# Kernel tuning notes

Measured on AMD Instinct MI355X. Metric: run time of the kernel, lower is better.

Reference implementation:

```python
import jax, jax.numpy as jnp
import numpy as np

B, N, C = 32, 256, 4096
H = 16
HEAD_DIM = C // H  # 256 == N, required by the module's math
SCALE = HEAD_DIM ** -0.5


def setup_inputs() -> dict:
    key = jax.random.key(0)
    ks = jax.random.split(key, 7)
    std = C ** -0.5
    return {
        "x1": jax.random.normal(ks[0], (B, N, C), dtype=jnp.float32),
        "x2": jax.random.normal(ks[1], (B, N, C), dtype=jnp.float32),
        "Wq": jax.random.normal(ks[2], (C, C), dtype=jnp.float32) * std,
        "Wk": jax.random.normal(ks[3], (C, C), dtype=jnp.float32) * std,
        "Wv": jax.random.normal(ks[4], (C, C), dtype=jnp.float32) * std,
        "Wp": jax.random.normal(ks[5], (C, C), dtype=jnp.float32) * std,
        "bp": jnp.zeros((C,), dtype=jnp.float32),
    }


def reference(x1, x2, Wq, Wk, Wv, Wp, bp):
    b, n, c = x1.shape
    h, hd = H, HEAD_DIM
    # QKV projections (qkv_bias=False); q pre-scaled as in source
    q = (x1 @ Wq.T) * SCALE
    k = x2 @ Wk.T
    v = x2 @ Wv.T
    split = lambda t: t.reshape(b, n, h, hd).transpose(0, 2, 1, 3)  # b h n hd
    q, k, v = split(q), split(k), split(v)
    # channel-wise attention: q^T @ k over the token axis -> [b, h, hd, hd]
    attn = jax.nn.softmax(jnp.einsum("bhni,bhnj->bhij", q, k), axis=-1)
    # attn @ v: inner dim of attn (hd) contracts with token axis of v (n == hd)
    out = jnp.einsum("bhin,bhnc->bhic", attn, v)  # [b, h, hd, hd]
    out = out.transpose(0, 2, 1, 3).reshape(b, n, c)
    x = out @ Wp.T + bp
    return (x, attn)
```

## Files before the change

### kernel.cpp

```cpp
#include <hip/hip_runtime.h>

typedef __attribute__((ext_vector_type(4))) float f32x4;
typedef __attribute__((ext_vector_type(8))) short short8;
typedef __attribute__((ext_vector_type(4))) unsigned short ushort4v;

__device__ __forceinline__ unsigned short rne_bf16(float f) {
  unsigned int u = __builtin_bit_cast(unsigned int, f);
  u += 0x7FFFu + ((u >> 16) & 1u);
  return (unsigned short)(u >> 16);
}

__device__ __forceinline__ void async16(void* lds, const void* g) {
  __builtin_amdgcn_global_load_lds(
      (const __attribute__((address_space(1))) void*)g,
      (__attribute__((address_space(3))) void*)lds, 16, 0, 0);
}

__device__ __forceinline__ f32x4 mfma16(short8 a, short8 b, f32x4 c) {
  return __builtin_amdgcn_mfma_f32_16x16x32_bf16(a, b, c, 0, 0, 0);
}

__global__ __launch_bounds__(256) void cast_k(const float* __restrict__ in,
                                              unsigned short* __restrict__ out,
                                              int n4) {
  int stride = gridDim.x * 256;
  for (int i = blockIdx.x * 256 + threadIdx.x; i < n4; i += stride) {
    float4 v = ((const float4*)in)[i];
    ushort4v o = {rne_bf16(v.x), rne_bf16(v.y), rne_bf16(v.z), rne_bf16(v.w)};
    ((ushort4v*)out)[i] = o;
  }
}

template <int MODE>
__global__ __launch_bounds__(512, 2) void gemm256(const unsigned short* __restrict__ A,
                                                  const unsigned short* __restrict__ B,
                                                  float* __restrict__ outF,
                                                  unsigned short* __restrict__ outB,
                                                  const float* __restrict__ bias,
                                                  int K, int lda, int ldb,
                                                  float scale, int gx) {
  __shared__ unsigned short lds[65536];
  const int tid = threadIdx.x;
  const int lane = tid & 63;
  const int wid = tid >> 6;
  const int wm = wid >> 2;
  const int wn = wid & 3;
  int lin = blockIdx.x;
  lin = (lin & 7) * (gridDim.x >> 3) + (lin >> 3);
  const int bx = lin % gx;
  const int by = lin / gx;
  const int m0 = by * 256, n0 = bx * 256;
  const int NT = K >> 6;

  const int gsw8 = (((tid & 3) ^ ((tid >> 3) & 3))) * 8;
  const unsigned short* gA = A + (size_t)(m0 + (tid >> 2)) * lda + gsw8;
  const unsigned short* gB = B + (size_t)(n0 + (tid >> 2)) * ldb + gsw8;
  const size_t astep = (size_t)128 * lda;
  const size_t bstep = (size_t)128 * ldb;
  unsigned short* ld0 = &lds[tid * 8];

#define STG_A(kt, kh, bf) do { \
    const unsigned short* s_ = gA + (kt) + (kh) * 32; \
    unsigned short* d_ = ld0 + (bf) * 32768 + (kh) * 8192; \
    async16(d_, s_); async16(d_ + 4096, s_ + astep); } while (0)
#define STG_B(kt, kh, bf) do { \
    const unsigned short* s_ = gB + (kt) + (kh) * 32; \
    unsigned short* d_ = ld0 + 16384 + (bf) * 32768 + (kh) * 8192; \
    async16(d_, s_); async16(d_ + 4096, s_ + bstep); } while (0)

  const int rl = lane & 15;
  const int ch = (lane >> 4) ^ ((rl >> 1) & 3);
  const int aidx = wm * 4096 + rl * 32 + ch * 8;
  const int bidx = 16384 + wn * 2048 + rl * 32 + ch * 8;

  f32x4 acc[8][4];
#pragma unroll
  for (int r = 0; r < 8; ++r)
#pragma unroll
    for (int s = 0; s < 4; ++s) acc[r][s] = (f32x4){0.f, 0.f, 0.f, 0.f};

  STG_A(0, 0, 0); STG_B(0, 0, 0); STG_A(0, 1, 0); STG_B(0, 1, 0);
  if (NT > 1) {
    STG_A(64, 0, 1); STG_B(64, 0, 1); STG_A(64, 1, 1);
    asm volatile("s_waitcnt vmcnt(6)" ::: "memory");
  } else {
    asm volatile("s_waitcnt vmcnt(0)" ::: "memory");
  }
  __builtin_amdgcn_s_barrier();

  short8 af[8];
  for (int t = 0; t < NT; ++t) {
    const int bb = (t & 1) * 32768;
    {
      short8 b0 = *(const short8*)&lds[bb + bidx];
      short8 b1 = *(const short8*)&lds[bb + bidx + 512];
#pragma unroll
      for (int r = 0; r < 8; ++r) af[r] = *(const short8*)&lds[bb + aidx + r * 512];
      if (t + 1 < NT) STG_B((t + 1) * 64, 1, (t + 1) & 1);
      __builtin_amdgcn_s_barrier();
      asm volatile("s_waitcnt lgkmcnt(0)" ::: "memory");
      __builtin_amdgcn_s_setprio(1);
#pragma unroll
      for (int r = 0; r < 8; ++r) {
        acc[r][0] = mfma16(af[r], b0, acc[r][0]);
        acc[r][1] = mfma16(af[r], b1, acc[r][1]);
      }
      __builtin_amdgcn_s_setprio(0);
      __builtin_amdgcn_s_barrier();
    }
    {
      short8 b2 = *(const short8*)&lds[bb + bidx + 1024];
      short8 b3 = *(const short8*)&lds[bb + bidx + 1536];
      if (t + 2 < NT) STG_A((t + 2) * 64, 0, t & 1);
      __builtin_amdgcn_s_barrier();
      asm volatile("s_waitcnt lgkmcnt(0)" ::: "memory");
      __builtin_amdgcn_s_setprio(1);
#pragma unroll
      for (int r = 0; r < 8; ++r) {
        acc[r][2] = mfma16(af[r], b2, acc[r][2]);
        acc[r][3] = mfma16(af[r], b3, acc[r][3]);
      }
      __builtin_amdgcn_s_setprio(0);
      __builtin_amdgcn_s_barrier();
    }
    {
      short8 b0 = *(const short8*)&lds[bb + 8192 + bidx];
      short8 b1 = *(const short8*)&lds[bb + 8192 + bidx + 512];
#pragma unroll
      for (int r = 0; r < 8; ++r) af[r] = *(const short8*)&lds[bb + 8192 + aidx + r * 512];
      if (t + 2 < NT) STG_B((t + 2) * 64, 0, t & 1);
      __builtin_amdgcn_s_barrier();
      asm volatile("s_waitcnt lgkmcnt(0)" ::: "memory");
      __builtin_amdgcn_s_setprio(1);
#pragma unroll
      for (int r = 0; r < 8; ++r) {
        acc[r][0] = mfma16(af[r], b0, acc[r][0]);
        acc[r][1] = mfma16(af[r], b1, acc[r][1]);
      }
      __builtin_amdgcn_s_setprio(0);
      __builtin_amdgcn_s_barrier();
    }
    {
      short8 b2 = *(const short8*)&lds[bb + 8192 + bidx + 1024];
      short8 b3 = *(const short8*)&lds[bb + 8192 + bidx + 1536];
      if (t + 2 < NT) STG_A((t + 2) * 64, 1, t & 1);
      __builtin_amdgcn_s_barrier();
      asm volatile("s_waitcnt lgkmcnt(0)" ::: "memory");
      __builtin_amdgcn_s_setprio(1);
#pragma unroll
      for (int r = 0; r < 8; ++r) {
        acc[r][2] = mfma16(af[r], b2, acc[r][2]);
        acc[r][3] = mfma16(af[r], b3, acc[r][3]);
      }
      __builtin_amdgcn_s_setprio(0);
      if (t + 1 < NT) {
        if (t + 1 == NT - 1) asm volatile("s_waitcnt vmcnt(0)" ::: "memory");
        else                 asm volatile("s_waitcnt vmcnt(6)" ::: "memory");
      }
      __builtin_amdgcn_s_barrier();
    }
  }
#undef STG_A
#undef STG_B

  const int fcol = lane & 15;
  const int frow = (lane >> 4) * 4;
#pragma unroll
  for (int r = 0; r < 8; ++r) {
#pragma unroll
    for (int s = 0; s < 4; ++s) {
      f32x4 v = acc[r][s];
      const int m = m0 + wm * 128 + r * 16 + frow;
      const int n = n0 + wn * 64 + s * 16 + fcol;
      if (MODE == 0) {
        ushort4v p;
#pragma unroll
        for (int j = 0; j < 4; ++j) p[j] = rne_bf16(v[j] * scale);
        size_t d = ((size_t)((m >> 8) * 16 + (n >> 8))) * 65536 +
                   (size_t)(n & 255) * 256 + (m & 255);
        *(ushort4v*)&outB[d] = p;
      } else {
        float bv = bias[n];
#pragma unroll
        for (int j = 0; j < 4; ++j) outF[(size_t)(m + j) * 4096 + n] = v[j] + bv;
      }
    }
  }
}

template <int MODE>
__global__ __launch_bounds__(256) void gemm_bt(const unsigned short* __restrict__ Ab,
                                               const unsigned short* __restrict__ Bb,
                                               float* __restrict__ outF,
                                               unsigned short* __restrict__ outB,
                                               int K, int lda, int ldb) {
  __shared__ short Ash[128 * 32];
  __shared__ short Bsh[128 * 32];

  const int tid = threadIdx.x;
  const int lane = tid & 63;
  const int wid = tid >> 6;
  const int z = blockIdx.z;
  const int m0 = blockIdx.y * 128;
  const int n0 = blockIdx.x * 128;

  const unsigned short* A = Ab + (size_t)z * 65536;
  const unsigned short* B = Bb + (size_t)z * 65536;

  const int wm = (wid >> 1) * 64;
  const int wn = (wid & 1) * 64;
  const int fcol = lane & 15;
  const int kslot = (lane >> 4) * 8;

  f32x4 acc[4][4];
#pragma unroll
  for (int r = 0; r < 4; ++r)
#pragma unroll
    for (int s = 0; s < 4; ++s) acc[r][s] = (f32x4){0.f, 0.f, 0.f, 0.f};

  const int arow = tid >> 2;
  const int acol = (tid & 3) * 8;
  const unsigned short* gA = A + (size_t)(m0 + arow) * lda + acol;
  const unsigned short* gB = B + (size_t)(n0 + arow) * ldb + acol;
  short* lA = &Ash[tid * 8];
  short* lB = &Bsh[tid * 8];

  for (int kt = 0; kt < K; kt += 32) {
    __syncthreads();
    async16(lA, gA + kt);
    async16(lA + 2048, gA + (size_t)64 * lda + kt);
    async16(lB, gB + kt);
    async16(lB + 2048, gB + (size_t)64 * ldb + kt);
    __syncthreads();

    short8 a[4], b[4];
#pragma unroll
    for (int r = 0; r < 4; ++r)
      a[r] = *(const short8*)&Ash[(wm + r * 16 + fcol) * 32 + kslot];
#pragma unroll
    for (int s = 0; s < 4; ++s)
      b[s] = *(const short8*)&Bsh[(wn + s * 16 + fcol) * 32 + kslot];
#pragma unroll
    for (int r = 0; r < 4; ++r)
#pragma unroll
      for (int s = 0; s < 4; ++s)
        acc[r][s] = __builtin_amdgcn_mfma_f32_16x16x32_bf16(a[r], b[s], acc[r][s], 0, 0, 0);
  }

  const int frow = (lane >> 4) * 4;
#pragma unroll
  for (int r = 0; r < 4; ++r) {
#pragma unroll
    for (int s = 0; s < 4; ++s) {
      f32x4 v = acc[r][s];
      const int m = m0 + wm + r * 16 + frow;
      const int n = n0 + wn + s * 16 + fcol;
      if (MODE == 1) {
        float* C = outF + (size_t)z * 65536;
#pragma unroll
        for (int j = 0; j < 4; ++j) C[(size_t)(m + j) * 256 + n] = v[j];
      } else {
        size_t base = ((size_t)((z >> 4) * 256 + m)) * 4096 + (z & 15) * 256 + n;
#pragma unroll
        for (int j = 0; j < 4; ++j) outB[base + (size_t)j * 4096] = rne_bf16(v[j]);
      }
    }
  }
}

__global__ __launch_bounds__(256) void softmax_k(float* __restrict__ S,
                                                 unsigned short* __restrict__ P) {
  const int lane = threadIdx.x & 63;
  const size_t row = (size_t)blockIdx.x * 4 + (threadIdx.x >> 6);
  float4 x = *(const float4*)&S[row * 256 + lane * 4];
  float mx = fmaxf(fmaxf(x.x, x.y), fmaxf(x.z, x.w));
#pragma unroll
  for (int off = 32; off; off >>= 1) mx = fmaxf(mx, __shfl_xor(mx, off, 64));
  float e0 = __expf(x.x - mx), e1 = __expf(x.y - mx);
  float e2 = __expf(x.z - mx), e3 = __expf(x.w - mx);
  float s = e0 + e1 + e2 + e3;
#pragma unroll
  for (int off = 32; off; off >>= 1) s += __shfl_xor(s, off, 64);
  const float inv = 1.0f / s;
  e0 *= inv; e1 *= inv; e2 *= inv; e3 *= inv;
  *(float4*)&S[row * 256 + lane * 4] = make_float4(e0, e1, e2, e3);
  ushort4v ob = {rne_bf16(e0), rne_bf16(e1), rne_bf16(e2), rne_bf16(e3)};
  *(ushort4v*)&P[row * 256 + lane * 4] = ob;
}

extern "C" void kernel_launch(void* const* d_in, const int* in_sizes, int n_in,
                              void* d_out, int out_size, void* d_ws, size_t ws_size,
                              hipStream_t stream) {
  const float* x1 = (const float*)d_in[0];
  const float* x2 = (const float*)d_in[1];
  const float* Wq = (const float*)d_in[2];
  const float* Wk = (const float*)d_in[3];
  const float* Wv = (const float*)d_in[4];
  const float* Wp = (const float*)d_in[5];
  const float* bp = (const float*)d_in[6];

  float* outX = (float*)d_out;
  float* outA = outX + (size_t)33554432;

  unsigned short* Qt  = (unsigned short*)d_ws;
  unsigned short* Kt  = Qt + 33554432;
  unsigned short* Vt  = Kt + 33554432;
  unsigned short* x1b = Vt + 33554432;
  unsigned short* x2b = x1b + 33554432;
  unsigned short* Wb  = x2b + 33554432;

  const float SCALE = 0.0625f;

  cast_k<<<2048, 256, 0, stream>>>(x1, x1b, 8388608);
  cast_k<<<2048, 256, 0, stream>>>(x2, x2b, 8388608);

  cast_k<<<2048, 256, 0, stream>>>(Wq, Wb, 4194304);
  gemm256<0><<<512, 512, 0, stream>>>(x1b, Wb, nullptr, Qt, nullptr,
                                      4096, 4096, 4096, SCALE, 16);
  cast_k<<<2048, 256, 0, stream>>>(Wk, Wb, 4194304);
  gemm256<0><<<512, 512, 0, stream>>>(x2b, Wb, nullptr, Kt, nullptr,
                                      4096, 4096, 4096, 1.0f, 16);
  cast_k<<<2048, 256, 0, stream>>>(Wv, Wb, 4194304);
  gemm256<0><<<512, 512, 0, stream>>>(x2b, Wb, nullptr, Vt, nullptr,
                                      4096, 4096, 4096, 1.0f, 16);

  gemm_bt<1><<<dim3(2, 2, 512), 256, 0, stream>>>(Qt, Kt, outA, nullptr, 256, 256, 256);
  softmax_k<<<32768, 256, 0, stream>>>(outA, x1b);
  gemm_bt<2><<<dim3(2, 2, 512), 256, 0, stream>>>(x1b, Vt, nullptr, x2b, 256, 256, 256);

  cast_k<<<2048, 256, 0, stream>>>(Wp, Wb, 4194304);
  gemm256<3><<<512, 512, 0, stream>>>(x2b, Wb, outX, nullptr, bp,
                                      4096, 4096, 4096, 1.0f, 16);
}
```

Measured before the change: 1.342 ms.

## Restructure GEMM main loop into two 32-MFMA phases with B-fragment prefetch

The GEMM main loop now runs two phases per 64-wide K tile instead of four, each issuing 32 MFMAs over a full 8x4 accumulator block. B fragments are double-buffered in registers and the next tile's B is read ahead during the current phase. Global-to-LDS staging is merged into one per-half-tile macro that loads A and B together. This halves the number of barriers and lgkmcnt waits per tile and is meant to overlap LDS reads with MFMA work, at the cost of more live registers (an extra 8 short8 values), which could reduce occupancy or cause spills.

After: 1.323 ms. Within noise of the previous version (-1.4%).

```diff
diff --git a/kernel.cpp b/kernel.cpp
--- a/kernel.cpp
+++ b/kernel.cpp
@@ -59,109 +59,78 @@
   const size_t bstep = (size_t)128 * ldb;
   unsigned short* ld0 = &lds[tid * 8];
 
-#define STG_A(kt, kh, bf) do { \
-    const unsigned short* s_ = gA + (kt) + (kh) * 32; \
-    unsigned short* d_ = ld0 + (bf) * 32768 + (kh) * 8192; \
-    async16(d_, s_); async16(d_ + 4096, s_ + astep); } while (0)
-#define STG_B(kt, kh, bf) do { \
-    const unsigned short* s_ = gB + (kt) + (kh) * 32; \
-    unsigned short* d_ = ld0 + 16384 + (bf) * 32768 + (kh) * 8192; \
-    async16(d_, s_); async16(d_ + 4096, s_ + bstep); } while (0)
+#define STG(Q) do { \
+    const int kt_ = ((Q) >> 1) * 64 + ((Q) & 1) * 32; \
+    const int off_ = (((Q) >> 1) & 1) * 32768 + ((Q) & 1) * 8192; \
+    const unsigned short* sA_ = gA + kt_; \
+    unsigned short* dA_ = ld0 + off_; \
+    async16(dA_, sA_); async16(dA_ + 4096, sA_ + astep); \
+    const unsigned short* sB_ = gB + kt_; \
+    unsigned short* dB_ = ld0 + 16384 + off_; \
+    async16(dB_, sB_); async16(dB_ + 4096, sB_ + bstep); } while (0)
 
   const int rl = lane & 15;
   const int ch = (lane >> 4) ^ ((rl >> 1) & 3);
   const int aidx = wm * 4096 + rl * 32 + ch * 8;
   const int bidx = 16384 + wn * 2048 + rl * 32 + ch * 8;
 
+  short8 af[8], bf0[4], bf1[4];
+#define READ_A(base) do { \
+    _Pragma("unroll") \
+    for (int r_ = 0; r_ < 8; ++r_) af[r_] = *(const short8*)&lds[(base) + aidx + r_ * 512]; \
+  } while (0)
+#define READ_B(base, dst) do { \
+    _Pragma("unroll") \
+    for (int s_ = 0; s_ < 4; ++s_) dst[s_] = *(const short8*)&lds[(base) + bidx + s_ * 512]; \
+  } while (0)
+
   f32x4 acc[8][4];
 #pragma unroll
   for (int r = 0; r < 8; ++r)
 #pragma unroll
     for (int s = 0; s < 4; ++s) acc[r][s] = (f32x4){0.f, 0.f, 0.f, 0.f};
 
-  STG_A(0, 0, 0); STG_B(0, 0, 0); STG_A(0, 1, 0); STG_B(0, 1, 0);
-  if (NT > 1) {
-    STG_A(64, 0, 1); STG_B(64, 0, 1); STG_A(64, 1, 1);
-    asm volatile("s_waitcnt vmcnt(6)" ::: "memory");
-  } else {
-    asm volatile("s_waitcnt vmcnt(0)" ::: "memory");
-  }
+#define MFMA32(bfX) do { \
+    __builtin_amdgcn_s_setprio(1); \
+    _Pragma("unroll") \
+    for (int r_ = 0; r_ < 8; ++r_) \
+      _Pragma("unroll") \
+      for (int s_ = 0; s_ < 4; ++s_) acc[r_][s_] = mfma16(af[r_], bfX[s_], acc[r_][s_]); \
+    __builtin_amdgcn_s_setprio(0); \
+  } while (0)
+
+  STG(0); STG(1); STG(2);
+  asm volatile("s_waitcnt vmcnt(4)" ::: "memory");
   __builtin_amdgcn_s_barrier();
-
-  short8 af[8];
+  READ_B(0, bf0);
+
   for (int t = 0; t < NT; ++t) {
     const int bb = (t & 1) * 32768;
-    {
-      short8 b0 = *(const short8*)&lds[bb + bidx];
-      short8 b1 = *(const short8*)&lds[bb + bidx + 512];
-#pragma unroll
-      for (int r = 0; r < 8; ++r) af[r] = *(const short8*)&lds[bb + aidx + r * 512];
-      if (t + 1 < NT) STG_B((t + 1) * 64, 1, (t + 1) & 1);
-      __builtin_amdgcn_s_barrier();
-      asm volatile("s_waitcnt lgkmcnt(0)" ::: "memory");
-      __builtin_amdgcn_s_setprio(1);
-#pragma unroll
-      for (int r = 0; r < 8; ++r) {
-        acc[r][0] = mfma16(af[r], b0, acc[r][0]);
-        acc[r][1] = mfma16(af[r], b1, acc[r][1]);
-      }
-      __builtin_amdgcn_s_setprio(0);
+    READ_A(bb);
+    READ_B(bb + 8192, bf1);
+    if (t + 1 < NT) STG(2 * t + 3);
+    __builtin_amdgcn_sched_barrier(0);
+    MFMA32(bf0);
+    if (t + 1 < NT) asm volatile("s_waitcnt vmcnt(4)" ::: "memory");
+    else            asm volatile("s_waitcnt vmcnt(0)" ::: "memory");
+    __builtin_amdgcn_s_barrier();
+    READ_A(bb + 8192);
+    if (t + 1 < NT) {
+      READ_B(((t + 1) & 1) * 32768, bf0);
+      if (t + 2 < NT) STG(2 * t + 4);
+    }
+    __builtin_amdgcn_sched_barrier(0);
+    MFMA32(bf1);
+    if (t + 1 < NT) {
+      if (t + 2 < NT) asm volatile("s_waitcnt vmcnt(4)" ::: "memory");
+      else            asm volatile("s_waitcnt vmcnt(0)" ::: "memory");
       __builtin_amdgcn_s_barrier();
     }
-    {
-      short8 b2 = *(const short8*)&lds[bb + bidx + 1024];
-      short8 b3 = *(const short8*)&lds[bb + bidx + 1536];
-      if (t + 2 < NT) STG_A((t + 2) * 64, 0, t & 1);
-      __builtin_amdgcn_s_barrier();
-      asm volatile("s_waitcnt lgkmcnt(0)" ::: "memory");
-      __builtin_amdgcn_s_setprio(1);
-#pragma unroll
-      for (int r = 0; r < 8; ++r) {
-        acc[r][2] = mfma16(af[r], b2, acc[r][2]);
-        acc[r][3] = mfma16(af[r], b3, acc[r][3]);
-      }
-      __builtin_amdgcn_s_setprio(0);
-      __builtin_amdgcn_s_barrier();
-    }
-    {
-      short8 b0 = *(const short8*)&lds[bb + 8192 + bidx];
-      short8 b1 = *(const short8*)&lds[bb + 8192 + bidx + 512];
-#pragma unroll
-      for (int r = 0; r < 8; ++r) af[r] = *(const short8*)&lds[bb + 8192 + aidx + r * 512];
-      if (t + 2 < NT) STG_B((t + 2) * 64, 0, t & 1);
-      __builtin_amdgcn_s_barrier();
-      asm volatile("s_waitcnt lgkmcnt(0)" ::: "memory");
-      __builtin_amdgcn_s_setprio(1);
-#pragma unroll
-      for (int r = 0; r < 8; ++r) {
-        acc[r][0] = mfma16(af[r], b0, acc[r][0]);
-        acc[r][1] = mfma16(af[r], b1, acc[r][1]);
-      }
-      __builtin_amdgcn_s_setprio(0);
-      __builtin_amdgcn_s_barrier();
-    }
-    {
-      short8 b2 = *(const short8*)&lds[bb + 8192 + bidx + 1024];
-      short8 b3 = *(const short8*)&lds[bb + 8192 + bidx + 1536];
-      if (t + 2 < NT) STG_A((t + 2) * 64, 1, t & 1);
-      __builtin_amdgcn_s_barrier();
-      asm volatile("s_waitcnt lgkmcnt(0)" ::: "memory");
-      __builtin_amdgcn_s_setprio(1);
-#pragma unroll
-      for (int r = 0; r < 8; ++r) {
-        acc[r][2] = mfma16(af[r], b2, acc[r][2]);
-        acc[r][3] = mfma16(af[r], b3, acc[r][3]);
-      }
-      __builtin_amdgcn_s_setprio(0);
-      if (t + 1 < NT) {
-        if (t + 1 == NT - 1) asm volatile("s_waitcnt vmcnt(0)" ::: "memory");
-        else                 asm volatile("s_waitcnt vmcnt(6)" ::: "memory");
-      }
-      __builtin_amdgcn_s_barrier();
-    }
-  }
-#undef STG_A
-#undef STG_B
+  }
+#undef STG
+#undef READ_A
+#undef READ_B
+#undef MFMA32
 
   const int fcol = lane & 15;
   const int frow = (lane >> 4) * 4;
```
